# Kernel optimization log

Measured on AMD Instinct MI355X. Metric: run time of the kernel, lower is better.

Reference implementation:

```python
import jax, jax.numpy as jnp
import numpy as np

N = 65536          # nodes
E = 1_048_576      # edges (avg degree 16)
IN_DIM = 16        # input_irreps = 16x0e
OUT_DIM = 8        # output_irreps = 8x0e
S_MUL = 32         # hidden 0e multiplicity
V_MUL = 16         # hidden 1o multiplicity
HID = S_MUL + 3 * V_MUL  # 80
LAYERS = 3
DEG = 16.0


def fctp(feat, eattr, w1, w2, w3, w4):
    """FullyConnectedTensorProduct(hidden x '1x0e+1x1o' -> hidden) per edge.
    Paths: 0e*0e->0e, 1o*1o->0e (dot, CG 1/sqrt(3)), 0e*1o->1o, 1o*0e->1o.
    Path weights mix multiplicities; e3nn-style fan-in normalization."""
    s1 = feat[:, :S_MUL]                         # [E, 32]
    v1 = feat[:, S_MUL:].reshape(-1, V_MUL, 3)   # [E, 16, 3]
    s2 = eattr[:, 0]                             # [E]
    v2 = eattr[:, 1:4]                           # [E, 3]
    c = 1.0 / np.sqrt(2.0)  # two paths per output irrep
    out_s = c * (jnp.einsum('ea,e,ac->ec', s1, s2, w1) / np.sqrt(S_MUL)
                 + jnp.einsum('eak,ek,ac->ec', v1, v2, w2) / np.sqrt(3.0 * V_MUL))
    out_v = c * (jnp.einsum('ea,ek,ac->eck', s1, v2, w3) / np.sqrt(S_MUL)
                 + jnp.einsum('eak,e,ac->eck', v1, s2, w4) / np.sqrt(V_MUL))
    return jnp.concatenate([out_s, out_v.reshape(-1, 3 * V_MUL)], axis=-1)


def setup_inputs() -> dict:
    key = jax.random.key(0)
    ks = jax.random.split(key, 12)
    inp = {
        'x': jax.random.normal(ks[0], (N, IN_DIM), jnp.float32),
        'edge_index': jax.random.randint(ks[1], (2, E), 0, N, jnp.int64 if jax.config.jax_enable_x64 else jnp.int32),
        'edge_attr': jax.random.normal(ks[2], (E, 4), jnp.float32),
        'W_in': jax.random.normal(ks[3], (IN_DIM, HID), jnp.float32) / np.sqrt(IN_DIM),
        'b_in': jnp.zeros((HID,), jnp.float32),
        'tp_w1': jax.random.normal(ks[4], (LAYERS, S_MUL, S_MUL), jnp.float32),
        'tp_w2': jax.random.normal(ks[5], (LAYERS, V_MUL, S_MUL), jnp.float32),
        'tp_w3': jax.random.normal(ks[6], (LAYERS, S_MUL, V_MUL), jnp.float32),
        'tp_w4': jax.random.normal(ks[7], (LAYERS, V_MUL, V_MUL), jnp.float32),
        'W_out': jax.random.normal(ks[8], (HID, OUT_DIM), jnp.float32) / np.sqrt(HID),
        'b_out': jnp.zeros((OUT_DIM,), jnp.float32),
    }
    return inp


def reference(x, edge_index, edge_attr, W_in, b_in, tp_w1, tp_w2, tp_w3, tp_w4, W_out, b_out):
    src, dst = edge_index[0], edge_index[1]
    h = x @ W_in + b_in                                   # [N, 80]
    for l in range(LAYERS):
        m = fctp(h[src], edge_attr, tp_w1[l], tp_w2[l], tp_w3[l], tp_w4[l])  # [E, 80]
        h = jax.ops.segment_sum(m, dst, num_segments=N) / np.sqrt(DEG)       # [N, 80]
    h = jax.nn.relu(h)
    return h @ W_out + b_out                              # [N, 8]
```

## Files before the change

### kernel.cpp

```cpp
#include <hip/hip_runtime.h>

#define NN 65536
#define NE 1048576
#define HID 80

typedef unsigned int u32;
typedef unsigned short u16;
typedef unsigned long long u64;

__device__ __forceinline__ u16 f2bf(float f) {
  u32 u = __float_as_uint(f);
  u = (u + 0x7fffu + ((u >> 16) & 1u)) >> 16;
  return (u16)u;
}
__device__ __forceinline__ float bfhi(u32 packed) {
  return __uint_as_float(packed & 0xffff0000u);
}
__device__ __forceinline__ float bflo(u32 packed) {
  return __uint_as_float(packed << 16);
}

__global__ __launch_bounds__(256) void k_in(const float* __restrict__ x,
    const float* __restrict__ W, const float* __restrict__ b,
    u16* __restrict__ hmain, u16* __restrict__ htail) {
  int idx = blockIdx.x * 256 + threadIdx.x;
  if (idx >= NN * HID) return;
  int n = idx / HID, l = idx % HID;
  const float* xr = x + n * 16;
  float acc = b[l];
#pragma unroll
  for (int k = 0; k < 16; k++) acc += xr[k] * W[k * HID + l];
  u16 v = f2bf(acc);
  if (l < 64) hmain[(size_t)n * 64 + l] = v;
  else htail[(size_t)n * 16 + (l - 64)] = v;
}

__global__ __launch_bounds__(256) void k_hist(const int* __restrict__ dst,
    int* __restrict__ counts, int* __restrict__ rank) {
  int base = blockIdx.x * 2048 + threadIdx.x;
#pragma unroll
  for (int k = 0; k < 8; k++) {
    int idx = base + k * 256;
    rank[idx] = atomicAdd(&counts[dst[idx]], 1);
  }
}

__global__ __launch_bounds__(256) void k_scan1(const int* __restrict__ counts,
    int* __restrict__ offsets, int* __restrict__ blocksum) {
  __shared__ int sc[256];
  int t = threadIdx.x;
  int base = blockIdx.x * 1024 + t * 4;
  int p0 = (counts[base] + 7) & ~7;
  int p1 = (counts[base + 1] + 7) & ~7;
  int p2 = (counts[base + 2] + 7) & ~7;
  int p3 = (counts[base + 3] + 7) & ~7;
  int s = p0 + p1 + p2 + p3;
  sc[t] = s;
  __syncthreads();
  for (int d = 1; d < 256; d <<= 1) {
    int v = (t >= d) ? sc[t - d] : 0;
    __syncthreads();
    sc[t] += v;
    __syncthreads();
  }
  int excl = sc[t] - s;
  offsets[base] = excl;
  offsets[base + 1] = excl + p0;
  offsets[base + 2] = excl + p0 + p1;
  offsets[base + 3] = excl + p0 + p1 + p2;
  if (t == 255) blocksum[blockIdx.x] = sc[255];
}

__global__ __launch_bounds__(64) void k_scan2(int* __restrict__ blocksum,
                                              int* __restrict__ dcnt) {
  int t = threadIdx.x;
  if (blockIdx.x == 0) {
    int v = blocksum[t];
    int incl = v;
#pragma unroll
    for (int d = 1; d < 64; d <<= 1) {
      int o = __shfl_up(incl, d, 64);
      if (t >= d) incl += o;
    }
    blocksum[t] = incl - v;
  } else {
    if (t >= 16) return;
    int v = dcnt[t];
    int incl = v;
#pragma unroll
    for (int d = 1; d < 16; d <<= 1) {
      int o = __shfl_up(incl, d, 64);
      if (t >= d) incl += o;
    }
    dcnt[t] = incl - v;
  }
}

__global__ __launch_bounds__(256) void k_nbucket(const int* __restrict__ counts,
    int* __restrict__ dcnt, int* __restrict__ brank, int* __restrict__ bidx) {
  int n = blockIdx.x * 256 + threadIdx.x;
  int degp = (counts[n] + 7) & ~7;
  int b = 15 - min(degp >> 3, 15);
  int lane = threadIdx.x & 63;
  int base = 0;
#pragma unroll 1
  for (int bb = 0; bb < 16; bb++) {
    u64 m = __ballot(b == bb);
    if (b == bb) {
      int leader = __ffsll((long long)m) - 1;
      int lr = __popcll(m & ((lane == 63) ? ~0ull >> 1 : ((1ull << lane) - 1)));
      int bs = 0;
      if (lane == leader) bs = atomicAdd(&dcnt[bb], __popcll(m));
      bs = __shfl(bs, leader, 64);
      base = bs + lr;
    }
  }
  brank[n] = base;
  bidx[n] = b;
}

__global__ __launch_bounds__(256) void k_node_fin(int* __restrict__ offsets,
    const int* __restrict__ blocksum, const int* __restrict__ counts,
    uint4* __restrict__ erec, const int* __restrict__ dcnt,
    const int* __restrict__ brank, const int* __restrict__ bidx,
    int* __restrict__ nperm) {
  int n = blockIdx.x * 256 + threadIdx.x;
  int off = offsets[n] + blocksum[n >> 10];
  offsets[n] = off;
  int deg = counts[n];
  int degp = (deg + 7) & ~7;
  uint4 z = make_uint4(0u, 0u, 0u, 0u);
  for (int e = deg; e < degp; e++) erec[off + e] = z;
  nperm[dcnt[bidx[n]] + brank[n]] = n;
}

__global__ __launch_bounds__(256) void k_fill(const int* __restrict__ src,
    const int* __restrict__ dst, const float4* __restrict__ eattr,
    const int* __restrict__ offsets, const int* __restrict__ rank,
    uint4* __restrict__ erec) {
  int base = blockIdx.x * 2048 + threadIdx.x;
#pragma unroll
  for (int k = 0; k < 8; k++) {
    int idx = base + k * 256;
    int d = dst[idx];
    float4 ea = eattr[idx];
    int s = src[idx];
    u32 c01 = (u32)f2bf(ea.x) | ((u32)f2bf(ea.y) << 16);
    u32 c23 = (u32)f2bf(ea.z) | ((u32)f2bf(ea.w) << 16);
    int pos = offsets[d] + rank[idx];
    erec[pos] = make_uint4((u32)s, c01, c23, 0u);
  }
}

__global__ __launch_bounds__(128, 3) void k_msg(const u16* __restrict__ hmain,
    const u16* __restrict__ htail, u16* __restrict__ omain,
    u16* __restrict__ otail,
    const float* __restrict__ w1, const float* __restrict__ w2,
    const float* __restrict__ w3, const float* __restrict__ w4,
    const int* __restrict__ offsets, const int* __restrict__ counts,
    const int* __restrict__ nperm, const uint4* __restrict__ erec) {
  __shared__ float Rlds[8][4][81];
  int tid = threadIdx.x;
  const int q = tid >> 4;
  const int c = tid & 15;
  const int n = nperm[blockIdx.x * 8 + q];

  float R[4][5];
#pragma unroll
  for (int j = 0; j < 4; j++)
#pragma unroll
    for (int i = 0; i < 5; i++) R[j][i] = 0.f;

  const int start = offsets[n];
  const int degp = (counts[n] + 7) & ~7;
  const int B = degp >> 3;
  const uint2* hrow = (const uint2*)hmain + c;
  const u16* trow = htail + c;

  int i = 0;
  for (; i + 2 <= B; i += 2) {
    const int baseA = start + 8 * i;
    const int baseB = baseA + 8;
    uint4 rA[8], rB[8];
#pragma unroll
    for (int k = 0; k < 8; k++) rA[k] = erec[baseA + k];
#pragma unroll
    for (int k = 0; k < 8; k++) rB[k] = erec[baseB + k];
    uint2 hA[8], hB[8];
    u32 tA[8], tB[8];
#pragma unroll
    for (int k = 0; k < 8; k++) {
      size_t s16 = (size_t)rA[k].x * 16;
      hA[k] = hrow[s16];
      tA[k] = trow[s16];
    }
#pragma unroll
    for (int k = 0; k < 8; k++) {
      size_t s16 = (size_t)rB[k].x * 16;
      hB[k] = hrow[s16];
      tB[k] = trow[s16];
    }
#pragma unroll
    for (int k = 0; k < 8; k++) {
      float A0 = bflo(hA[k].x), A1 = bfhi(hA[k].x);
      float A2 = bflo(hA[k].y), A3 = bfhi(hA[k].y);
      float A4 = bflo(tA[k]);
      float f0 = bflo(rA[k].y), f1 = bfhi(rA[k].y);
      float f2 = bflo(rA[k].z), f3 = bfhi(rA[k].z);
      R[0][0] += f0 * A0; R[0][1] += f0 * A1; R[0][2] += f0 * A2;
      R[0][3] += f0 * A3; R[0][4] += f0 * A4;
      R[1][0] += f1 * A0; R[1][1] += f1 * A1; R[1][2] += f1 * A2;
      R[1][3] += f1 * A3; R[1][4] += f1 * A4;
      R[2][0] += f2 * A0; R[2][1] += f2 * A1; R[2][2] += f2 * A2;
      R[2][3] += f2 * A3; R[2][4] += f2 * A4;
      R[3][0] += f3 * A0; R[3][1] += f3 * A1; R[3][2] += f3 * A2;
      R[3][3] += f3 * A3; R[3][4] += f3 * A4;
    }
#pragma unroll
    for (int k = 0; k < 8; k++) {
      float A0 = bflo(hB[k].x), A1 = bfhi(hB[k].x);
      float A2 = bflo(hB[k].y), A3 = bfhi(hB[k].y);
      float A4 = bflo(tB[k]);
      float f0 = bflo(rB[k].y), f1 = bfhi(rB[k].y);
      float f2 = bflo(rB[k].z), f3 = bfhi(rB[k].z);
      R[0][0] += f0 * A0; R[0][1] += f0 * A1; R[0][2] += f0 * A2;
      R[0][3] += f0 * A3; R[0][4] += f0 * A4;
      R[1][0] += f1 * A0; R[1][1] += f1 * A1; R[1][2] += f1 * A2;
      R[1][3] += f1 * A3; R[1][4] += f1 * A4;
      R[2][0] += f2 * A0; R[2][1] += f2 * A1; R[2][2] += f2 * A2;
      R[2][3] += f2 * A3; R[2][4] += f2 * A4;
      R[3][0] += f3 * A0; R[3][1] += f3 * A1; R[3][2] += f3 * A2;
      R[3][3] += f3 * A3; R[3][4] += f3 * A4;
    }
  }
  if (i < B) {
    const int baseA = start + 8 * i;
    uint4 rA[8];
#pragma unroll
    for (int k = 0; k < 8; k++) rA[k] = erec[baseA + k];
    uint2 hA[8];
    u32 tA[8];
#pragma unroll
    for (int k = 0; k < 8; k++) {
      size_t s16 = (size_t)rA[k].x * 16;
      hA[k] = hrow[s16];
      tA[k] = trow[s16];
    }
#pragma unroll
    for (int k = 0; k < 8; k++) {
      float A0 = bflo(hA[k].x), A1 = bfhi(hA[k].x);
      float A2 = bflo(hA[k].y), A3 = bfhi(hA[k].y);
      float A4 = bflo(tA[k]);
      float f0 = bflo(rA[k].y), f1 = bfhi(rA[k].y);
      float f2 = bflo(rA[k].z), f3 = bfhi(rA[k].z);
      R[0][0] += f0 * A0; R[0][1] += f0 * A1; R[0][2] += f0 * A2;
      R[0][3] += f0 * A3; R[0][4] += f0 * A4;
      R[1][0] += f1 * A0; R[1][1] += f1 * A1; R[1][2] += f1 * A2;
      R[1][3] += f1 * A3; R[1][4] += f1 * A4;
      R[2][0] += f2 * A0; R[2][1] += f2 * A1; R[2][2] += f2 * A2;
      R[2][3] += f2 * A3; R[2][4] += f2 * A4;
      R[3][0] += f3 * A0; R[3][1] += f3 * A1; R[3][2] += f3 * A2;
      R[3][3] += f3 * A3; R[3][4] += f3 * A4;
    }
  }

#pragma unroll
  for (int j = 0; j < 4; j++) {
#pragma unroll
    for (int k = 0; k < 4; k++) Rlds[q][j][4 * c + k] = R[j][k];
    Rlds[q][j][64 + c] = R[j][4];
  }

  const float C1 = 0.03125f;
  const float C2 = 0.025515518f;
  const float C3 = 0.03125f;
  const float C4 = 0.044194174f;

  u16* opm = omain + (size_t)n * 64;

  float s0 = 0.f, s1 = 0.f;
#pragma unroll
  for (int a = 0; a < 32; a++) {
    float rs = Rlds[q][0][a];
    s0 += rs * w1[a * 32 + c];
    s1 += rs * w1[a * 32 + c + 16];
  }
  float t0 = 0.f, t1 = 0.f;
#pragma unroll
  for (int a = 0; a < 16; a++) {
    float T = Rlds[q][1][32 + 3 * a] + Rlds[q][2][33 + 3 * a] +
              Rlds[q][3][34 + 3 * a];
    t0 += T * w2[a * 32 + c];
    t1 += T * w2[a * 32 + c + 16];
  }
  opm[c] = f2bf(C1 * s0 + C2 * t0);
  opm[c + 16] = f2bf(C1 * s1 + C2 * t1);

#pragma unroll
  for (int v2 = 0; v2 < 3; v2++) {
    int c2 = 32 + 16 * v2 + c;
    int cv = (c2 - 32) / 3, k = (c2 - 32) % 3;
    float a3 = 0.f, a4 = 0.f;
#pragma unroll
    for (int a = 0; a < 32; a++) a3 += Rlds[q][k + 1][a] * w3[a * 16 + cv];
#pragma unroll
    for (int a = 0; a < 16; a++)
      a4 += Rlds[q][0][32 + 3 * a + k] * w4[a * 16 + cv];
    u16 v = f2bf(C3 * a3 + C4 * a4);
    if (v2 < 2) opm[32 + 16 * v2 + c] = v;
    else otail[(size_t)n * 16 + c] = v;
  }
}

__global__ __launch_bounds__(256) void k_out(const u16* __restrict__ hmain,
    const u16* __restrict__ htail, const float* __restrict__ W,
    const float* __restrict__ b, float* __restrict__ out) {
  int idx = blockIdx.x * 256 + threadIdx.x;
  if (idx >= NN * 8) return;
  int n = idx >> 3, c = idx & 7;
  const uint2* hr = (const uint2*)(hmain + (size_t)n * 64);
  const u32* tr = (const u32*)(htail + (size_t)n * 16);
  float acc = b[c];
#pragma unroll
  for (int cc = 0; cc < 16; cc++) {
    uint2 v = hr[cc];
    float v0 = bflo(v.x), v1 = bfhi(v.x), v2 = bflo(v.y), v3 = bfhi(v.y);
    v0 = v0 > 0.f ? v0 : 0.f;
    v1 = v1 > 0.f ? v1 : 0.f;
    v2 = v2 > 0.f ? v2 : 0.f;
    v3 = v3 > 0.f ? v3 : 0.f;
    acc += v0 * W[(4 * cc) * 8 + c] + v1 * W[(4 * cc + 1) * 8 + c] +
           v2 * W[(4 * cc + 2) * 8 + c] + v3 * W[(4 * cc + 3) * 8 + c];
  }
#pragma unroll
  for (int k = 0; k < 8; k++) {
    u32 v = tr[k];
    float v0 = bflo(v), v1 = bfhi(v);
    v0 = v0 > 0.f ? v0 : 0.f;
    v1 = v1 > 0.f ? v1 : 0.f;
    acc += v0 * W[(64 + 2 * k) * 8 + c] + v1 * W[(64 + 2 * k + 1) * 8 + c];
  }
  out[idx] = acc;
}

extern "C" void kernel_launch(void* const* d_in, const int* in_sizes, int n_in,
                              void* d_out, int out_size, void* d_ws,
                              size_t ws_size, hipStream_t stream) {
  const float* x = (const float*)d_in[0];
  const int* ei = (const int*)d_in[1];
  const float* eattr = (const float*)d_in[2];
  const float* W_in = (const float*)d_in[3];
  const float* b_in = (const float*)d_in[4];
  const float* tp_w1 = (const float*)d_in[5];
  const float* tp_w2 = (const float*)d_in[6];
  const float* tp_w3 = (const float*)d_in[7];
  const float* tp_w4 = (const float*)d_in[8];
  const float* W_out = (const float*)d_in[9];
  const float* b_out = (const float*)d_in[10];
  float* out = (float*)d_out;

  char* ws = (char*)d_ws;
  size_t off = 0;
  auto alloc = [&](size_t bytes) {
    void* p = ws + off;
    off += (bytes + 255) & ~size_t(255);
    return p;
  };
  const size_t NEP = (size_t)NE + 8 * (size_t)NN;
  u16* hm_a = (u16*)alloc((size_t)NN * 64 * 2);
  u16* ht_a = (u16*)alloc((size_t)NN * 16 * 2);
  u16* hm_b = (u16*)alloc((size_t)NN * 64 * 2);
  u16* ht_b = (u16*)alloc((size_t)NN * 16 * 2);
  int* counts = (int*)alloc((size_t)NN * 4);
  int* offsets = (int*)alloc((size_t)NN * 4);
  int* blocksum = (int*)alloc(64 * 4);
  int* rank = (int*)alloc((size_t)NE * 4);
  int* dcnt = (int*)alloc(16 * 4);
  int* brank = (int*)alloc((size_t)NN * 4);
  int* bidx = (int*)alloc((size_t)NN * 4);
  int* nperm = (int*)alloc((size_t)NN * 4);
  uint4* erec = (uint4*)alloc(NEP * 16);

  const int* src = ei;
  const int* dst = ei + NE;

  hipMemsetAsync(counts, 0, (size_t)NN * 4, stream);
  hipMemsetAsync(dcnt, 0, 16 * 4, stream);
  k_in<<<(NN * HID + 255) / 256, 256, 0, stream>>>(x, W_in, b_in, hm_a, ht_a);
  k_hist<<<NE / 2048, 256, 0, stream>>>(dst, counts, rank);
  k_nbucket<<<NN / 256, 256, 0, stream>>>(counts, dcnt, brank, bidx);
  k_scan1<<<64, 256, 0, stream>>>(counts, offsets, blocksum);
  k_scan2<<<2, 64, 0, stream>>>(blocksum, dcnt);
  k_node_fin<<<NN / 256, 256, 0, stream>>>(offsets, blocksum, counts, erec,
                                           dcnt, brank, bidx, nperm);
  k_fill<<<NE / 2048, 256, 0, stream>>>(src, dst, (const float4*)eattr,
                                        offsets, rank, erec);

  u16* hmi = hm_a;
  u16* hti = ht_a;
  u16* hmo = hm_b;
  u16* hto = ht_b;
  for (int l = 0; l < 3; l++) {
    k_msg<<<NN / 8, 128, 0, stream>>>(hmi, hti, hmo, hto, tp_w1 + l * 1024,
                                      tp_w2 + l * 512, tp_w3 + l * 512,
                                      tp_w4 + l * 256, offsets, counts, nperm,
                                      erec);
    u16* t;
    t = hmi; hmi = hmo; hmo = t;
    t = hti; hti = hto; hto = t;
  }
  k_out<<<(NN * 8 + 255) / 256, 256, 0, stream>>>(hmi, hti, W_out, b_out, out);
}
```

Before: 394.6 us.

## Split edge records into u16 src and bf16 attrs, fuse output head and prep kernels

Replaces the 16-byte edge record with a 2-byte u16 source index plus an 8-byte attribute pair, cutting the edge-stream bytes read in each message layer. The final message layer applies the ReLU and output projection in-kernel through a shuffle reduction, so the separate output kernel and the final hidden-state write are dropped. The bucket and scan preprocessing kernels are merged, and the dcnt memset moves into k_hist. Storing the source as u16 only works because N is 65536, so indices 0..65535 fit exactly; the dcnt zeroing in k_hist also needs to be ordered correctly with respect to the nbucket atomics.

```diff
diff --git a/kernel.cpp b/kernel.cpp
--- a/kernel.cpp
+++ b/kernel.cpp
@@ -36,7 +36,8 @@
 }
 
 __global__ __launch_bounds__(256) void k_hist(const int* __restrict__ dst,
-    int* __restrict__ counts, int* __restrict__ rank) {
+    int* __restrict__ counts, int* __restrict__ rank, int* __restrict__ dcnt) {
+  if (blockIdx.x == 0 && threadIdx.x < 16) dcnt[threadIdx.x] = 0;
   int base = blockIdx.x * 2048 + threadIdx.x;
 #pragma unroll
   for (int k = 0; k < 8; k++) {
@@ -45,30 +46,53 @@
   }
 }
 
-__global__ __launch_bounds__(256) void k_scan1(const int* __restrict__ counts,
-    int* __restrict__ offsets, int* __restrict__ blocksum) {
+__global__ __launch_bounds__(256) void k_nb_scan(const int* __restrict__ counts,
+    int* __restrict__ offsets, int* __restrict__ blocksum,
+    int* __restrict__ dcnt, int* __restrict__ brank, int* __restrict__ bidx) {
   __shared__ int sc[256];
   int t = threadIdx.x;
-  int base = blockIdx.x * 1024 + t * 4;
-  int p0 = (counts[base] + 7) & ~7;
-  int p1 = (counts[base + 1] + 7) & ~7;
-  int p2 = (counts[base + 2] + 7) & ~7;
-  int p3 = (counts[base + 3] + 7) & ~7;
-  int s = p0 + p1 + p2 + p3;
-  sc[t] = s;
-  __syncthreads();
-  for (int d = 1; d < 256; d <<= 1) {
-    int v = (t >= d) ? sc[t - d] : 0;
+  if (blockIdx.x < 64) {
+    int base = blockIdx.x * 1024 + t * 4;
+    int p0 = (counts[base] + 7) & ~7;
+    int p1 = (counts[base + 1] + 7) & ~7;
+    int p2 = (counts[base + 2] + 7) & ~7;
+    int p3 = (counts[base + 3] + 7) & ~7;
+    int s = p0 + p1 + p2 + p3;
+    sc[t] = s;
     __syncthreads();
-    sc[t] += v;
-    __syncthreads();
-  }
-  int excl = sc[t] - s;
-  offsets[base] = excl;
-  offsets[base + 1] = excl + p0;
-  offsets[base + 2] = excl + p0 + p1;
-  offsets[base + 3] = excl + p0 + p1 + p2;
-  if (t == 255) blocksum[blockIdx.x] = sc[255];
+    for (int d = 1; d < 256; d <<= 1) {
+      int v = (t >= d) ? sc[t - d] : 0;
+      __syncthreads();
+      sc[t] += v;
+      __syncthreads();
+    }
+    int excl = sc[t] - s;
+    offsets[base] = excl;
+    offsets[base + 1] = excl + p0;
+    offsets[base + 2] = excl + p0 + p1;
+    offsets[base + 3] = excl + p0 + p1 + p2;
+    if (t == 255) blocksum[blockIdx.x] = sc[255];
+  } else {
+    int n = (blockIdx.x - 64) * 256 + t;
+    int degp = (counts[n] + 7) & ~7;
+    int b = 15 - min(degp >> 3, 15);
+    int lane = t & 63;
+    int base = 0;
+#pragma unroll 1
+    for (int bb = 0; bb < 16; bb++) {
+      u64 m = __ballot(b == bb);
+      if (b == bb) {
+        int leader = __ffsll((long long)m) - 1;
+        int lr = __popcll(m & ((lane == 63) ? ~0ull >> 1 : ((1ull << lane) - 1)));
+        int bs = 0;
+        if (lane == leader) bs = atomicAdd(&dcnt[bb], __popcll(m));
+        bs = __shfl(bs, leader, 64);
+        base = bs + lr;
+      }
+    }
+    brank[n] = base;
+    bidx[n] = b;
+  }
 }
 
 __global__ __launch_bounds__(64) void k_scan2(int* __restrict__ blocksum,
@@ -96,48 +120,28 @@
   }
 }
 
-__global__ __launch_bounds__(256) void k_nbucket(const int* __restrict__ counts,
-    int* __restrict__ dcnt, int* __restrict__ brank, int* __restrict__ bidx) {
-  int n = blockIdx.x * 256 + threadIdx.x;
-  int degp = (counts[n] + 7) & ~7;
-  int b = 15 - min(degp >> 3, 15);
-  int lane = threadIdx.x & 63;
-  int base = 0;
-#pragma unroll 1
-  for (int bb = 0; bb < 16; bb++) {
-    u64 m = __ballot(b == bb);
-    if (b == bb) {
-      int leader = __ffsll((long long)m) - 1;
-      int lr = __popcll(m & ((lane == 63) ? ~0ull >> 1 : ((1ull << lane) - 1)));
-      int bs = 0;
-      if (lane == leader) bs = atomicAdd(&dcnt[bb], __popcll(m));
-      bs = __shfl(bs, leader, 64);
-      base = bs + lr;
-    }
-  }
-  brank[n] = base;
-  bidx[n] = b;
-}
-
 __global__ __launch_bounds__(256) void k_node_fin(int* __restrict__ offsets,
     const int* __restrict__ blocksum, const int* __restrict__ counts,
-    uint4* __restrict__ erec, const int* __restrict__ dcnt,
-    const int* __restrict__ brank, const int* __restrict__ bidx,
-    int* __restrict__ nperm) {
+    u16* __restrict__ esrc, uint2* __restrict__ eat,
+    const int* __restrict__ dcnt, const int* __restrict__ brank,
+    const int* __restrict__ bidx, int* __restrict__ nperm) {
   int n = blockIdx.x * 256 + threadIdx.x;
   int off = offsets[n] + blocksum[n >> 10];
   offsets[n] = off;
   int deg = counts[n];
   int degp = (deg + 7) & ~7;
-  uint4 z = make_uint4(0u, 0u, 0u, 0u);
-  for (int e = deg; e < degp; e++) erec[off + e] = z;
+  uint2 z2 = make_uint2(0u, 0u);
+  for (int e = deg; e < degp; e++) {
+    esrc[off + e] = 0;
+    eat[off + e] = z2;
+  }
   nperm[dcnt[bidx[n]] + brank[n]] = n;
 }
 
 __global__ __launch_bounds__(256) void k_fill(const int* __restrict__ src,
     const int* __restrict__ dst, const float4* __restrict__ eattr,
     const int* __restrict__ offsets, const int* __restrict__ rank,
-    uint4* __restrict__ erec) {
+    u16* __restrict__ esrc, uint2* __restrict__ eat) {
   int base = blockIdx.x * 2048 + threadIdx.x;
 #pragma unroll
   for (int k = 0; k < 8; k++) {
@@ -148,17 +152,21 @@
     u32 c01 = (u32)f2bf(ea.x) | ((u32)f2bf(ea.y) << 16);
     u32 c23 = (u32)f2bf(ea.z) | ((u32)f2bf(ea.w) << 16);
     int pos = offsets[d] + rank[idx];
-    erec[pos] = make_uint4((u32)s, c01, c23, 0u);
-  }
-}
-
+    esrc[pos] = (u16)s;
+    eat[pos] = make_uint2(c01, c23);
+  }
+}
+
+template <int LAST>
 __global__ __launch_bounds__(128, 3) void k_msg(const u16* __restrict__ hmain,
     const u16* __restrict__ htail, u16* __restrict__ omain,
     u16* __restrict__ otail,
     const float* __restrict__ w1, const float* __restrict__ w2,
     const float* __restrict__ w3, const float* __restrict__ w4,
     const int* __restrict__ offsets, const int* __restrict__ counts,
-    const int* __restrict__ nperm, const uint4* __restrict__ erec) {
+    const int* __restrict__ nperm, const u16* __restrict__ esrc,
+    const uint2* __restrict__ eat, const float* __restrict__ Wout,
+    const float* __restrict__ bout, float* __restrict__ outp) {
   __shared__ float Rlds[8][4][81];
   int tid = threadIdx.x;
   const int q = tid >> 4;
@@ -181,22 +189,27 @@
   for (; i + 2 <= B; i += 2) {
     const int baseA = start + 8 * i;
     const int baseB = baseA + 8;
-    uint4 rA[8], rB[8];
-#pragma unroll
-    for (int k = 0; k < 8; k++) rA[k] = erec[baseA + k];
-#pragma unroll
-    for (int k = 0; k < 8; k++) rB[k] = erec[baseB + k];
+    u32 sA[8], sB[8];
+    uint2 aA[8], aB[8];
+#pragma unroll
+    for (int k = 0; k < 8; k++) sA[k] = esrc[baseA + k];
+#pragma unroll
+    for (int k = 0; k < 8; k++) aA[k] = eat[baseA + k];
+#pragma unroll
+    for (int k = 0; k < 8; k++) sB[k] = esrc[baseB + k];
+#pragma unroll
+    for (int k = 0; k < 8; k++) aB[k] = eat[baseB + k];
     uint2 hA[8], hB[8];
     u32 tA[8], tB[8];
 #pragma unroll
     for (int k = 0; k < 8; k++) {
-      size_t s16 = (size_t)rA[k].x * 16;
+      size_t s16 = (size_t)sA[k] * 16;
       hA[k] = hrow[s16];
       tA[k] = trow[s16];
     }
 #pragma unroll
     for (int k = 0; k < 8; k++) {
-      size_t s16 = (size_t)rB[k].x * 16;
+      size_t s16 = (size_t)sB[k] * 16;
       hB[k] = hrow[s16];
       tB[k] = trow[s16];
     }
@@ -205,8 +218,8 @@
       float A0 = bflo(hA[k].x), A1 = bfhi(hA[k].x);
       float A2 = bflo(hA[k].y), A3 = bfhi(hA[k].y);
       float A4 = bflo(tA[k]);
-      float f0 = bflo(rA[k].y), f1 = bfhi(rA[k].y);
-      float f2 = bflo(rA[k].z), f3 = bfhi(rA[k].z);
+      float f0 = bflo(aA[k].x), f1 = bfhi(aA[k].x);
+      float f2 = bflo(aA[k].y), f3 = bfhi(aA[k].y);
       R[0][0] += f0 * A0; R[0][1] += f0 * A1; R[0][2] += f0 * A2;
       R[0][3] += f0 * A3; R[0][4] += f0 * A4;
       R[1][0] += f1 * A0; R[1][1] += f1 * A1; R[1][2] += f1 * A2;
@@ -221,8 +234,8 @@
       float A0 = bflo(hB[k].x), A1 = bfhi(hB[k].x);
       float A2 = bflo(hB[k].y), A3 = bfhi(hB[k].y);
       float A4 = bflo(tB[k]);
-      float f0 = bflo(rB[k].y), f1 = bfhi(rB[k].y);
-      float f2 = bflo(rB[k].z), f3 = bfhi(rB[k].z);
+      float f0 = bflo(aB[k].x), f1 = bfhi(aB[k].x);
+      float f2 = bflo(aB[k].y), f3 = bfhi(aB[k].y);
       R[0][0] += f0 * A0; R[0][1] += f0 * A1; R[0][2] += f0 * A2;
       R[0][3] += f0 * A3; R[0][4] += f0 * A4;
       R[1][0] += f1 * A0; R[1][1] += f1 * A1; R[1][2] += f1 * A2;
@@ -235,14 +248,17 @@
   }
   if (i < B) {
     const int baseA = start + 8 * i;
-    uint4 rA[8];
-#pragma unroll
-    for (int k = 0; k < 8; k++) rA[k] = erec[baseA + k];
+    u32 sA[8];
+    uint2 aA[8];
+#pragma unroll
+    for (int k = 0; k < 8; k++) sA[k] = esrc[baseA + k];
+#pragma unroll
+    for (int k = 0; k < 8; k++) aA[k] = eat[baseA + k];
     uint2 hA[8];
     u32 tA[8];
 #pragma unroll
     for (int k = 0; k < 8; k++) {
-      size_t s16 = (size_t)rA[k].x * 16;
+      size_t s16 = (size_t)sA[k] * 16;
       hA[k] = hrow[s16];
       tA[k] = trow[s16];
     }
@@ -251,8 +267,8 @@
       float A0 = bflo(hA[k].x), A1 = bfhi(hA[k].x);
       float A2 = bflo(hA[k].y), A3 = bfhi(hA[k].y);
       float A4 = bflo(tA[k]);
-      float f0 = bflo(rA[k].y), f1 = bfhi(rA[k].y);
-      float f2 = bflo(rA[k].z), f3 = bfhi(rA[k].z);
+      float f0 = bflo(aA[k].x), f1 = bfhi(aA[k].x);
+      float f2 = bflo(aA[k].y), f3 = bfhi(aA[k].y);
       R[0][0] += f0 * A0; R[0][1] += f0 * A1; R[0][2] += f0 * A2;
       R[0][3] += f0 * A3; R[0][4] += f0 * A4;
       R[1][0] += f1 * A0; R[1][1] += f1 * A1; R[1][2] += f1 * A2;
@@ -293,8 +309,22 @@
     t0 += T * w2[a * 32 + c];
     t1 += T * w2[a * 32 + c + 16];
   }
-  opm[c] = f2bf(C1 * s0 + C2 * t0);
-  opm[c + 16] = f2bf(C1 * s1 + C2 * t1);
+
+  float y[8];
+  if (LAST) {
+#pragma unroll
+    for (int j = 0; j < 8; j++) y[j] = 0.f;
+    float vs0 = C1 * s0 + C2 * t0;
+    float vs1 = C1 * s1 + C2 * t1;
+    vs0 = vs0 > 0.f ? vs0 : 0.f;
+    vs1 = vs1 > 0.f ? vs1 : 0.f;
+#pragma unroll
+    for (int j = 0; j < 8; j++)
+      y[j] += vs0 * Wout[c * 8 + j] + vs1 * Wout[(c + 16) * 8 + j];
+  } else {
+    opm[c] = f2bf(C1 * s0 + C2 * t0);
+    opm[c + 16] = f2bf(C1 * s1 + C2 * t1);
+  }
 
 #pragma unroll
   for (int v2 = 0; v2 < 3; v2++) {
@@ -306,41 +336,30 @@
 #pragma unroll
     for (int a = 0; a < 16; a++)
       a4 += Rlds[q][0][32 + 3 * a + k] * w4[a * 16 + cv];
-    u16 v = f2bf(C3 * a3 + C4 * a4);
-    if (v2 < 2) opm[32 + 16 * v2 + c] = v;
-    else otail[(size_t)n * 16 + c] = v;
-  }
-}
-
-__global__ __launch_bounds__(256) void k_out(const u16* __restrict__ hmain,
-    const u16* __restrict__ htail, const float* __restrict__ W,
-    const float* __restrict__ b, float* __restrict__ out) {
-  int idx = blockIdx.x * 256 + threadIdx.x;
-  if (idx >= NN * 8) return;
-  int n = idx >> 3, c = idx & 7;
-  const uint2* hr = (const uint2*)(hmain + (size_t)n * 64);
-  const u32* tr = (const u32*)(htail + (size_t)n * 16);
-  float acc = b[c];
-#pragma unroll
-  for (int cc = 0; cc < 16; cc++) {
-    uint2 v = hr[cc];
-    float v0 = bflo(v.x), v1 = bfhi(v.x), v2 = bflo(v.y), v3 = bfhi(v.y);
-    v0 = v0 > 0.f ? v0 : 0.f;
-    v1 = v1 > 0.f ? v1 : 0.f;
-    v2 = v2 > 0.f ? v2 : 0.f;
-    v3 = v3 > 0.f ? v3 : 0.f;
-    acc += v0 * W[(4 * cc) * 8 + c] + v1 * W[(4 * cc + 1) * 8 + c] +
-           v2 * W[(4 * cc + 2) * 8 + c] + v3 * W[(4 * cc + 3) * 8 + c];
-  }
-#pragma unroll
-  for (int k = 0; k < 8; k++) {
-    u32 v = tr[k];
-    float v0 = bflo(v), v1 = bfhi(v);
-    v0 = v0 > 0.f ? v0 : 0.f;
-    v1 = v1 > 0.f ? v1 : 0.f;
-    acc += v0 * W[(64 + 2 * k) * 8 + c] + v1 * W[(64 + 2 * k + 1) * 8 + c];
-  }
-  out[idx] = acc;
+    float val = C3 * a3 + C4 * a4;
+    if (LAST) {
+      val = val > 0.f ? val : 0.f;
+#pragma unroll
+      for (int j = 0; j < 8; j++) y[j] += val * Wout[c2 * 8 + j];
+    } else {
+      u16 v = f2bf(val);
+      if (v2 < 2) opm[32 + 16 * v2 + c] = v;
+      else otail[(size_t)n * 16 + c] = v;
+    }
+  }
+
+  if (LAST) {
+#pragma unroll
+    for (int m = 1; m <= 8; m <<= 1) {
+#pragma unroll
+      for (int j = 0; j < 8; j++) y[j] += __shfl_xor(y[j], m, 64);
+    }
+    float w = y[0];
+#pragma unroll
+    for (int j = 1; j < 8; j++)
+      if (c == j) w = y[j];
+    if (c < 8) outp[(size_t)n * 8 + c] = w + bout[c];
+  }
 }
 
 extern "C" void kernel_launch(void* const* d_in, const int* in_sizes, int n_in,
@@ -379,35 +398,38 @@
   int* brank = (int*)alloc((size_t)NN * 4);
   int* bidx = (int*)alloc((size_t)NN * 4);
   int* nperm = (int*)alloc((size_t)NN * 4);
-  uint4* erec = (uint4*)alloc(NEP * 16);
+  u16* esrc = (u16*)alloc(NEP * 2);
+  uint2* eat = (uint2*)alloc(NEP * 8);
 
   const int* src = ei;
   const int* dst = ei + NE;
 
   hipMemsetAsync(counts, 0, (size_t)NN * 4, stream);
-  hipMemsetAsync(dcnt, 0, 16 * 4, stream);
   k_in<<<(NN * HID + 255) / 256, 256, 0, stream>>>(x, W_in, b_in, hm_a, ht_a);
-  k_hist<<<NE / 2048, 256, 0, stream>>>(dst, counts, rank);
-  k_nbucket<<<NN / 256, 256, 0, stream>>>(counts, dcnt, brank, bidx);
-  k_scan1<<<64, 256, 0, stream>>>(counts, offsets, blocksum);
+  k_hist<<<NE / 2048, 256, 0, stream>>>(dst, counts, rank, dcnt);
+  k_nb_scan<<<64 + NN / 256, 256, 0, stream>>>(counts, offsets, blocksum, dcnt,
+                                               brank, bidx);
   k_scan2<<<2, 64, 0, stream>>>(blocksum, dcnt);
-  k_node_fin<<<NN / 256, 256, 0, stream>>>(offsets, blocksum, counts, erec,
-                                           dcnt, brank, bidx, nperm);
+  k_node_fin<<<NN / 256, 256, 0, stream>>>(offsets, blocksum, counts, esrc,
+                                           eat, dcnt, brank, bidx, nperm);
   k_fill<<<NE / 2048, 256, 0, stream>>>(src, dst, (const float4*)eattr,
-                                        offsets, rank, erec);
+                                        offsets, rank, esrc, eat);
 
   u16* hmi = hm_a;
   u16* hti = ht_a;
   u16* hmo = hm_b;
   u16* hto = ht_b;
-  for (int l = 0; l < 3; l++) {
-    k_msg<<<NN / 8, 128, 0, stream>>>(hmi, hti, hmo, hto, tp_w1 + l * 1024,
-                                      tp_w2 + l * 512, tp_w3 + l * 512,
-                                      tp_w4 + l * 256, offsets, counts, nperm,
-                                      erec);
+  for (int l = 0; l < 2; l++) {
+    k_msg<0><<<NN / 8, 128, 0, stream>>>(hmi, hti, hmo, hto, tp_w1 + l * 1024,
+                                         tp_w2 + l * 512, tp_w3 + l * 512,
+                                         tp_w4 + l * 256, offsets, counts,
+                                         nperm, esrc, eat, W_out, b_out, out);
     u16* t;
     t = hmi; hmi = hmo; hmo = t;
     t = hti; hti = hto; hto = t;
   }
-  k_out<<<(NN * 8 + 255) / 256, 256, 0, stream>>>(hmi, hti, W_out, b_out, out);
-}
+  k_msg<1><<<NN / 8, 128, 0, stream>>>(hmi, hti, hmo, hto, tp_w1 + 2048,
+                                       tp_w2 + 1024, tp_w3 + 1024, tp_w4 + 512,
+                                       offsets, counts, nperm, esrc, eat,
+                                       W_out, b_out, out);
+}
```

Result: no change. 393.1 us (-0.4%).
